# Kernel optimization log

Measured on AMD Instinct MI355X. Metric: run time of the kernel, lower is better.

The kernel has to match this reference:

```python
import math
import jax, jax.numpy as jnp
import numpy as np

B, IB, S, D = 8, 1024, 4096, 512
WINDOW = 1
SPARSITY = 2


def setup_inputs() -> dict:
    key = jax.random.key(0)
    ks = jax.random.split(key, 12)
    std = 1.0 / math.sqrt(D)
    std_b2s = 1.0 / math.sqrt(IB)
    return {
        "text_feature": jax.random.normal(ks[0], (B, S, D), jnp.float32),
        "image_feature": jax.random.normal(ks[1], (B, IB, D), jnp.float32),
        "Wq": jax.random.normal(ks[2], (D, D), jnp.float32) * std,
        "bq": jax.random.normal(ks[3], (D,), jnp.float32) * std,
        "Wk": jax.random.normal(ks[4], (D, D), jnp.float32) * std,
        "bk": jax.random.normal(ks[5], (D,), jnp.float32) * std,
        "Wv": jax.random.normal(ks[6], (D, D), jnp.float32) * std,
        "bv": jax.random.normal(ks[7], (D,), jnp.float32) * std,
        # torch Linear(in=IB, out=S): weight shape (S, IB)
        "Wb2s": jax.random.normal(ks[8], (S, IB), jnp.float32) * std_b2s,
        "bb2s": jax.random.normal(ks[9], (S,), jnp.float32) * std_b2s,
    }


def _banded_softmax_weights():
    # attention_mask[i, max(0,i-w):min(S,i+w+1)] = 1 ; since IB < S this is a
    # banded 0/1 matrix over (IB, IB), then row-softmax.
    i = jnp.arange(IB)[:, None]
    j = jnp.arange(IB)[None, :]
    mask = ((j >= i - WINDOW) & (j <= i + WINDOW)).astype(jnp.float32)
    return jax.nn.softmax(mask, axis=-1)  # (IB, IB)


def reference(text_feature, image_feature, Wq, bq, Wk, bk, Wv, bv, Wb2s, bb2s):
    d_k = text_feature.shape[-1]
    q = image_feature @ Wq.T + bq            # (B, IB, D)
    k = text_feature @ Wk.T + bk              # (B, S, D)
    v = text_feature @ Wv.T + bv              # (B, S, D)

    # batch-invariant sparse attention pattern: compute once, broadcast via einsum
    aw = _banded_softmax_weights()             # (IB, IB)
    aw = aw @ Wb2s.T + bb2s                    # (IB, S)
    num_nonzero = S // SPARSITY + 2 * WINDOW
    topk_scores, topk_idx = jax.lax.top_k(aw, num_nonzero)  # (IB, nnz)
    sparse = jnp.zeros((IB, S), aw.dtype).at[jnp.arange(IB)[:, None], topk_idx].set(topk_scores)

    out = jnp.einsum('is,bsd->bid', sparse, k)                       # (B, IB, D)
    out = jnp.einsum('bid,bjd->bij', q, out) / math.sqrt(d_k)        # (B, IB, IB)
    out = out @ Wb2s.T + bb2s                                        # (B, IB, S)
    out = jnp.einsum('bis,bsd->bid', jax.nn.softmax(out, axis=-1), v)  # (B, IB, D)
    return out
```

## Files before the change

### kernel.cpp

```cpp
#include <hip/hip_runtime.h>

#define B_  8
#define IB_ 1024
#define S_  4096
#define D_  512

typedef _Float16 f16;
typedef _Float16 f16x8 __attribute__((ext_vector_type(8)));
typedef _Float16 f16x4 __attribute__((ext_vector_type(4)));
typedef float    f32x4 __attribute__((ext_vector_type(4)));

__device__ __forceinline__ void gld_lds16(const f16* g, f16* l) {
  __builtin_amdgcn_global_load_lds(
      (const __attribute__((address_space(1))) void*)g,
      (__attribute__((address_space(3))) void*)l, 16, 0, 0);
}

__global__ __launch_bounds__(256) void gemm_bt(
    const f16* __restrict__ A, const f16* __restrict__ B,
    float* __restrict__ C32, f16* __restrict__ C16,
    int M, int N, int K, int lda, int ldb, int ksplit,
    long long sAb, long long sBb, long long sCb,
    const float* __restrict__ bias_row, const float* __restrict__ bias_col,
    float scale)
{
  __shared__ f16 ldsA[2][128 * 32];
  __shared__ f16 ldsB[2][128 * 32];
  const int tid  = threadIdx.x;
  const int lane = tid & 63;
  const int wave = tid >> 6;
  const int zb   = blockIdx.z / ksplit;
  const int ks   = blockIdx.z % ksplit;
  A += (size_t)zb * (size_t)sAb;
  B += (size_t)zb * (size_t)sBb;
  const int m0 = blockIdx.y * 128;
  const int n0 = blockIdx.x * 128;
  const int wm = wave >> 1, wn = wave & 1;

  f32x4 acc[4][4];
#pragma unroll
  for (int i = 0; i < 4; ++i)
#pragma unroll
    for (int j = 0; j < 4; ++j) acc[i][j] = (f32x4){0.f, 0.f, 0.f, 0.f};

  int aoff[4], boff[4];
  const int cl = lane >> 4;
#pragma unroll
  for (int r = 0; r < 4; ++r) {
    int rowa = wm * 64 + r * 16 + (lane & 15);
    aoff[r] = rowa * 32 + (cl ^ ((rowa >> 1) & 3)) * 8;
    int rowb = wn * 64 + r * 16 + (lane & 15);
    boff[r] = rowb * 32 + (cl ^ ((rowb >> 1) & 3)) * 8;
  }
  int srow[2], scg[2];
#pragma unroll
  for (int it = 0; it < 2; ++it) {
    int ch = wave * 64 + it * 256 + lane;
    srow[it] = ch >> 2;
    scg[it]  = (ch & 3) ^ ((srow[it] >> 1) & 3);
  }

#define STAGE(bf_, k0_)                                                        \
  do {                                                                         \
    _Pragma("unroll")                                                          \
    for (int it = 0; it < 2; ++it) {                                           \
      gld_lds16(A + (size_t)(m0 + srow[it]) * (size_t)lda +                    \
                    ((k0_) + scg[it] * 8),                                     \
                &ldsA[bf_][(wave * 64 + it * 256) * 8]);                       \
      gld_lds16(B + (size_t)(n0 + srow[it]) * (size_t)ldb +                    \
                    ((k0_) + scg[it] * 8),                                     \
                &ldsB[bf_][(wave * 64 + it * 256) * 8]);                       \
    }                                                                          \
  } while (0)

  const int Kc   = K / ksplit;
  const int kbeg = ks * Kc;
  const int nt   = Kc / 32;

  STAGE(0, kbeg);
  for (int t = 0; t < nt; ++t) {
    const int cur = t & 1;
    if (t + 1 < nt) {
      STAGE(cur ^ 1, kbeg + (t + 1) * 32);
      asm volatile("s_waitcnt vmcnt(4)" ::: "memory");
    } else {
      asm volatile("s_waitcnt vmcnt(0)" ::: "memory");
    }
    __builtin_amdgcn_s_barrier();
    __builtin_amdgcn_sched_barrier(0);
    f16x8 af[4], bf[4];
#pragma unroll
    for (int r = 0; r < 4; ++r) af[r] = *(const f16x8*)&ldsA[cur][aoff[r]];
#pragma unroll
    for (int r = 0; r < 4; ++r) bf[r] = *(const f16x8*)&ldsB[cur][boff[r]];
#pragma unroll
    for (int mr = 0; mr < 4; ++mr)
#pragma unroll
      for (int nr = 0; nr < 4; ++nr)
        acc[mr][nr] = __builtin_amdgcn_mfma_f32_16x16x32_f16(
            af[mr], bf[nr], acc[mr][nr], 0, 0, 0);
    __builtin_amdgcn_sched_barrier(0);
    __builtin_amdgcn_s_barrier();
    __builtin_amdgcn_sched_barrier(0);
  }
#undef STAGE

  const size_t cz = (ksplit > 1) ? (size_t)blockIdx.z : (size_t)zb;
  float* c32 = C32 ? C32 + cz * (size_t)sCb : nullptr;
  f16*   c16 = C16 ? C16 + cz * (size_t)sCb : nullptr;
#pragma unroll
  for (int mr = 0; mr < 4; ++mr) {
#pragma unroll
    for (int r = 0; r < 4; ++r) {
      int grow = m0 + wm * 64 + mr * 16 + (lane >> 4) * 4 + r;
      float brv = bias_row ? bias_row[grow] : 0.f;
#pragma unroll
      for (int nr = 0; nr < 4; ++nr) {
        int gcol = n0 + wn * 64 + nr * 16 + (lane & 15);
        float v = acc[mr][nr][r] * scale + brv +
                  (bias_col ? bias_col[gcol] : 0.f);
        if (c32) c32[(size_t)grow * N + gcol] = v;
        else     c16[(size_t)grow * N + gcol] = (f16)v;
      }
    }
  }
}

__global__ __launch_bounds__(256) void gemm_pt(
    const f16* __restrict__ Bt, const float* __restrict__ uarr,
    const float* __restrict__ inv2, const float* __restrict__ Acs,
    const float* __restrict__ bb2s, f16* __restrict__ parts)
{
  __shared__ f16 ldsB[2][128 * 32];
  __shared__ float cA[1024], cB[1024];
  const int tid  = threadIdx.x;
  const int lane = tid & 63;
  const int wave = tid >> 6;
  int id = (int)blockIdx.x;
  id = (id & 7) * 128 + (id >> 3);
  const int x  = id & 3;
  const int y  = (id >> 2) & 7;
  const int z  = id >> 5;
  const int zb = z >> 2, ks = z & 3;
  const int kbeg = ks * 1024;
  const int m0 = y * 128, n0 = x * 128;
  const int wm = wave >> 1, wn = wave & 1;
  const f16* B = Bt + (size_t)zb * ((size_t)D_ * S_);

  for (int i = tid; i < 1024; i += 256) {
    cA[i] = Acs[kbeg + i];
    cB[i] = bb2s[kbeg + i];
  }
  const int cl = lane >> 4;
  float u_[4], iv_[4];
#pragma unroll
  for (int r = 0; r < 4; ++r) {
    int row = zb * IB_ + m0 + wm * 64 + r * 16 + (lane & 15);
    u_[r]  = uarr[row];
    iv_[r] = inv2[row];
  }
  int boff[4];
#pragma unroll
  for (int r = 0; r < 4; ++r) {
    int rowb = wn * 64 + r * 16 + (lane & 15);
    boff[r] = rowb * 32 + (cl ^ ((rowb >> 1) & 3)) * 8;
  }
  int srow[2], scg[2];
#pragma unroll
  for (int it = 0; it < 2; ++it) {
    int ch = wave * 64 + it * 256 + lane;
    srow[it] = ch >> 2;
    scg[it]  = (ch & 3) ^ ((srow[it] >> 1) & 3);
  }
  f32x4 acc[4][4];
#pragma unroll
  for (int i = 0; i < 4; ++i)
#pragma unroll
    for (int j = 0; j < 4; ++j) acc[i][j] = (f32x4){0.f, 0.f, 0.f, 0.f};

#define STAGEB(bf_, k0_)                                                       \
  do {                                                                         \
    _Pragma("unroll")                                                          \
    for (int it = 0; it < 2; ++it) {                                           \
      gld_lds16(B + (size_t)(n0 + srow[it]) * (size_t)S_ +                     \
                    ((k0_) + scg[it] * 8),                                     \
                &ldsB[bf_][(wave * 64 + it * 256) * 8]);                       \
    }                                                                          \
  } while (0)

  __syncthreads();
  STAGEB(0, kbeg);
  for (int t = 0; t < 32; ++t) {
    const int cur = t & 1;
    if (t + 1 < 32) STAGEB(cur ^ 1, kbeg + (t + 1) * 32);
    const int kl = t * 32 + cl * 8;
    float a8[8], b8[8];
#pragma unroll
    for (int j = 0; j < 8; ++j) { a8[j] = cA[kl + j]; b8[j] = cB[kl + j]; }
    f16x8 af[4];
#pragma unroll
    for (int r = 0; r < 4; ++r)
#pragma unroll
      for (int j = 0; j < 8; ++j)
        af[r][j] = (f16)(__expf(fmaf(u_[r], a8[j], b8[j])) * iv_[r]);
    if (t + 1 < 32) asm volatile("s_waitcnt vmcnt(2)" ::: "memory");
    else            asm volatile("s_waitcnt vmcnt(0)" ::: "memory");
    __builtin_amdgcn_s_barrier();
    __builtin_amdgcn_sched_barrier(0);
    f16x8 bf[4];
#pragma unroll
    for (int r = 0; r < 4; ++r) bf[r] = *(const f16x8*)&ldsB[cur][boff[r]];
#pragma unroll
    for (int mr = 0; mr < 4; ++mr)
#pragma unroll
      for (int nr = 0; nr < 4; ++nr)
        acc[mr][nr] = __builtin_amdgcn_mfma_f32_16x16x32_f16(
            af[mr], bf[nr], acc[mr][nr], 0, 0, 0);
    __builtin_amdgcn_sched_barrier(0);
    __builtin_amdgcn_s_barrier();
    __builtin_amdgcn_sched_barrier(0);
  }
#undef STAGEB

  f16* cp = parts + (size_t)z * (size_t)(IB_ * D_);
#pragma unroll
  for (int mr = 0; mr < 4; ++mr) {
#pragma unroll
    for (int rr = 0; rr < 4; ++rr) {
      int grow = m0 + wm * 64 + mr * 16 + (lane >> 4) * 4 + rr;
#pragma unroll
      for (int nr = 0; nr < 4; ++nr) {
        int gcol = n0 + wn * 64 + nr * 16 + (lane & 15);
        cp[(size_t)grow * D_ + gcol] = (f16)acc[mr][nr][rr];
      }
    }
  }
}

__global__ __launch_bounds__(256) void reduce_ks4_f16(
    const f16x8* __restrict__ p, f16x8* __restrict__ o, unsigned n8)
{
  const unsigned pb8 = (IB_ * D_) / 8;
  unsigned i = blockIdx.x * 256u + threadIdx.x;
  const unsigned stride = gridDim.x * 256u;
  for (; i < n8; i += stride) {
    unsigned g = i / pb8, r = i - g * pb8;
    size_t base = ((size_t)g * 4u) * pb8 + r;
    float acc[8] = {0.f, 0.f, 0.f, 0.f, 0.f, 0.f, 0.f, 0.f};
#pragma unroll
    for (int ks = 0; ks < 4; ++ks) {
      f16x8 v = p[base + (size_t)ks * pb8];
#pragma unroll
      for (int j = 0; j < 8; ++j) acc[j] += (float)v[j];
    }
    f16x8 h;
#pragma unroll
    for (int j = 0; j < 8; ++j) h[j] = (f16)acc[j];
    o[i] = h;
  }
}

__global__ __launch_bounds__(256) void reduce_ks2_bias(
    const f16x8* __restrict__ p, const float* __restrict__ bias,
    float4* __restrict__ o, unsigned n8)
{
  unsigned i = blockIdx.x * 256u + threadIdx.x;
  const unsigned stride = gridDim.x * 256u;
  for (; i < n8; i += stride) {
    f16x8 a = p[i];
    f16x8 b = p[i + (size_t)n8];
    const int c0 = (int)((i * 8u) & (D_ - 1));
    float4 lo, hi;
    lo.x = (float)a[0] + (float)b[0] + bias[c0 + 0];
    lo.y = (float)a[1] + (float)b[1] + bias[c0 + 1];
    lo.z = (float)a[2] + (float)b[2] + bias[c0 + 2];
    lo.w = (float)a[3] + (float)b[3] + bias[c0 + 3];
    hi.x = (float)a[4] + (float)b[4] + bias[c0 + 4];
    hi.y = (float)a[5] + (float)b[5] + bias[c0 + 5];
    hi.z = (float)a[6] + (float)b[6] + bias[c0 + 6];
    hi.w = (float)a[7] + (float)b[7] + bias[c0 + 7];
    o[(size_t)i * 2]     = lo;
    o[(size_t)i * 2 + 1] = hi;
  }
}

__global__ __launch_bounds__(256) void cvt_f32_to_f16(
    const float* __restrict__ in, f16* __restrict__ out, unsigned n)
{
  unsigned i = (blockIdx.x * 256u + threadIdx.x) * 4u;
  if (i >= n) return;
  const float4 v = *(const float4*)(in + i);
  f16x4 h;
  h[0] = (f16)v.x; h[1] = (f16)v.y; h[2] = (f16)v.z; h[3] = (f16)v.w;
  *(f16x4*)(out + i) = h;
}

__global__ __launch_bounds__(256) void transpose_text(
    const float* __restrict__ in, f16* __restrict__ out)
{
  __shared__ float t[32][65];
  const int b = blockIdx.z;
  const int s0 = blockIdx.x * 64, d0 = blockIdx.y * 32;
  const int dx = threadIdx.x & 31;
  const int sy = threadIdx.x >> 5;
  const float* ip = in + ((size_t)b * S_ + s0) * D_ + d0;
#pragma unroll
  for (int j = 0; j < 8; ++j) {
    int sl = j * 8 + sy;
    t[dx][sl] = ip[(size_t)sl * D_ + dx];
  }
  __syncthreads();
  const int sx = threadIdx.x & 63;
  const int dy = threadIdx.x >> 6;
  f16* op = out + ((size_t)b * D_ + d0) * S_ + s0;
#pragma unroll
  for (int j = 0; j < 8; ++j) {
    int dl = j * 4 + dy;
    op[(size_t)dl * S_ + sx] = (f16)t[dl][sx];
  }
}

__global__ __launch_bounds__(256) void rowsum_kernel(
    const float* __restrict__ W, float* __restrict__ out)
{
  int s = blockIdx.x;
  const float* row = W + (size_t)s * IB_;
  float acc = 0.f;
  for (int j = threadIdx.x; j < IB_; j += 256) acc += row[j];
  __shared__ float red[4];
#pragma unroll
  for (int o = 32; o >= 1; o >>= 1) acc += __shfl_xor(acc, o);
  if ((threadIdx.x & 63) == 0) red[threadIdx.x >> 6] = acc;
  __syncthreads();
  if (threadIdx.x == 0) out[s] = red[0] + red[1] + red[2] + red[3];
}

__device__ __forceinline__ unsigned fkey(float x) {
  unsigned u = __float_as_uint(x);
  return (u & 0x80000000u) ? ~u : (u | 0x80000000u);
}

__global__ __launch_bounds__(256) void prep_mu(
    const float* __restrict__ Acs, const float* __restrict__ bb2s,
    float* __restrict__ muk, float* __restrict__ rhat)
{
  __shared__ float vals[S_];
  __shared__ unsigned hist[256];
  __shared__ unsigned sprefix;
  __shared__ int srem;
  __shared__ float rred[4];
  const float e1 = 2.71828182845904523536f;
  const float Z = 3.f * e1 + (float)(IB_ - 3);
  const float alpha = 1.f / Z;
  for (int s = threadIdx.x; s < S_; s += 256)
    vals[s] = alpha * Acs[s] + bb2s[s];
  if (threadIdx.x == 0) { sprefix = 0u; srem = S_ / 2 + 2; }
  __syncthreads();
  for (int shift = 24; shift >= 0; shift -= 8) {
    hist[threadIdx.x] = 0u;
    __syncthreads();
    unsigned pfx = sprefix;
    unsigned himask = (shift == 24) ? 0u : (0xFFFFFFFFu << (shift + 8));
    for (int s = threadIdx.x; s < S_; s += 256) {
      unsigned key = fkey(vals[s]);
      if ((key & himask) == (pfx & himask))
        atomicAdd(&hist[(key >> shift) & 255u], 1u);
    }
    __syncthreads();
    if (threadIdx.x == 0) {
      int rem = srem;
      unsigned acc = 0;
      int b = 255;
      for (; b > 0; --b) {
        unsigned c = hist[b];
        if (acc + c >= (unsigned)rem) break;
        acc += c;
      }
      sprefix = pfx | ((unsigned)b << shift);
      srem = rem - (int)acc;
    }
    __syncthreads();
  }
  const unsigned T = sprefix;
  float myrs = 0.f;
  for (int s = threadIdx.x; s < S_; s += 256) {
    float v = vals[s];
    bool keep = fkey(v) >= T;
    muk[s] = keep ? v : 0.f;
    if (keep) myrs += v;
  }
#pragma unroll
  for (int o = 32; o >= 1; o >>= 1) myrs += __shfl_xor(myrs, o);
  if ((threadIdx.x & 63) == 0) rred[threadIdx.x >> 6] = myrs;
  __syncthreads();
  if (threadIdx.x == 0) rhat[0] = rred[0] + rred[1] + rred[2] + rred[3];
}

__global__ __launch_bounds__(256) void that_partial(
    const float* __restrict__ text, const float* __restrict__ muk,
    float* __restrict__ tp)
{
  const int d = blockIdx.x * 256 + threadIdx.x;
  const int c = blockIdx.y;
  const int b = blockIdx.z;
  const float* tb = text + ((size_t)b * S_ + (size_t)c * 128) * D_ + d;
  float acc = 0.f;
  for (int s = 0; s < 128; ++s) {
    float m = muk[c * 128 + s];
    if (m != 0.f) acc += m * tb[(size_t)s * D_];
  }
  tp[((size_t)b * 32 + c) * D_ + d] = acc;
}

__global__ __launch_bounds__(256) void tt_reduce(
    const float* __restrict__ tp, float* __restrict__ tt)
{
  const int d = blockIdx.x * 256 + threadIdx.x;
  const int b = blockIdx.y;
  float acc = 0.f;
#pragma unroll
  for (int c = 0; c < 32; ++c) acc += tp[((size_t)b * 32 + c) * D_ + d];
  tt[(size_t)b * D_ + d] = acc;
}

__global__ __launch_bounds__(256) void mhat2_kernel(
    const float* __restrict__ tt, const float* __restrict__ Wk,
    const float* __restrict__ bk, const float* __restrict__ rhat,
    float* __restrict__ mh)
{
  __shared__ float tl[B_ * D_];
  const int t = threadIdx.x;
  for (int i = t; i < B_ * D_; i += 256) tl[i] = tt[i];
  __syncthreads();
  const int r = blockIdx.x;
  const int lane = t & 63, wave = t >> 6;
  const float* wr = Wk + (size_t)r * D_;
  float w[8];
#pragma unroll
  for (int j = 0; j < 8; ++j) w[j] = wr[lane + 64 * j];
  const float bkr = bk[r] * rhat[0];
#pragma unroll
  for (int bb = 0; bb < 2; ++bb) {
    const int b = wave * 2 + bb;
    float acc = 0.f;
#pragma unroll
    for (int j = 0; j < 8; ++j) acc += w[j] * tl[b * D_ + lane + 64 * j];
#pragma unroll
    for (int o = 32; o >= 1; o >>= 1) acc += __shfl_xor(acc, o);
    if (lane == 0) mh[b * D_ + r] = acc + bkr;
  }
}

__global__ __launch_bounds__(256) void ypart_kernel(
    const float* __restrict__ Wq, const float* __restrict__ mh,
    float* __restrict__ yp)
{
  __shared__ float ms[B_ * 64];
  const int t = threadIdx.x;
  const int d = blockIdx.x * 256 + t;
  const int c = blockIdx.y;
  for (int i = t; i < B_ * 64; i += 256) {
    int b = i >> 6, rr = i & 63;
    ms[i] = mh[b * D_ + c * 64 + rr];
  }
  __syncthreads();
  float acc[8] = {0.f, 0.f, 0.f, 0.f, 0.f, 0.f, 0.f, 0.f};
  for (int rr = 0; rr < 64; ++rr) {
    float wv = Wq[(size_t)(c * 64 + rr) * D_ + d];
#pragma unroll
    for (int b = 0; b < 8; ++b) acc[b] += wv * ms[b * 64 + rr];
  }
#pragma unroll
  for (int b = 0; b < 8; ++b)
    yp[((size_t)c * 8 + b) * D_ + d] = acc[b];
}

__global__ __launch_bounds__(256) void yred_kernel(
    const float* __restrict__ yp, float* __restrict__ y)
{
  const int d = blockIdx.x * 256 + threadIdx.x;
  const int b = blockIdx.y;
  float acc = 0.f;
#pragma unroll
  for (int c = 0; c < 8; ++c) acc += yp[((size_t)c * 8 + b) * D_ + d];
  y[(size_t)b * D_ + d] = acc;
}

__global__ __launch_bounds__(256) void cb_kernel(
    const float* __restrict__ bq, const float* __restrict__ mh,
    float* __restrict__ cb)
{
  const int lane = threadIdx.x & 63, wave = threadIdx.x >> 6;
#pragma unroll
  for (int bb = 0; bb < 2; ++bb) {
    const int b = wave * 2 + bb;
    float acc = 0.f;
#pragma unroll
    for (int j = 0; j < 8; ++j) {
      int k = lane + 64 * j;
      acc += bq[k] * mh[b * D_ + k];
    }
#pragma unroll
    for (int o = 32; o >= 1; o >>= 1) acc += __shfl_xor(acc, o);
    if (lane == 0) cb[b] = acc;
  }
}

__global__ __launch_bounds__(256) void u_kernel(
    const float* __restrict__ img, const float* __restrict__ y,
    const float* __restrict__ cb, float scl, float* __restrict__ u)
{
  const int lane = threadIdx.x & 63, wave = threadIdx.x >> 6;
  const int row = blockIdx.x * 4 + wave;
  const int b = row >> 10;
  const float* ir = img + (size_t)row * D_;
  const float* yb = y + (size_t)b * D_;
  float acc = 0.f;
#pragma unroll
  for (int j = 0; j < 8; ++j) {
    int d = lane + 64 * j;
    acc += ir[d] * yb[d];
  }
#pragma unroll
  for (int o = 32; o >= 1; o >>= 1) acc += __shfl_xor(acc, o);
  if (lane == 0) u[row] = (acc + cb[b]) * scl;
}

__global__ __launch_bounds__(256) void pstat_kernel(
    const float* __restrict__ uarr, const float* __restrict__ Acs,
    const float* __restrict__ bb2s, float* __restrict__ inv2)
{
  const int row = blockIdx.x;
  const int t = threadIdx.x;
  __shared__ float red[4];
  const float u = uarr[row];
  float v[16];
  float mx = -3.4e38f;
#pragma unroll
  for (int j = 0; j < 16; ++j) {
    int s = t + 256 * j;
    v[j] = fmaf(u, Acs[s], bb2s[s]);
    mx = fmaxf(mx, v[j]);
  }
#pragma unroll
  for (int o = 32; o >= 1; o >>= 1) mx = fmaxf(mx, __shfl_xor(mx, o));
  if ((t & 63) == 0) red[t >> 6] = mx;
  __syncthreads();
  mx = fmaxf(fmaxf(red[0], red[1]), fmaxf(red[2], red[3]));
  __syncthreads();
  float sum = 0.f;
#pragma unroll
  for (int j = 0; j < 16; ++j) sum += __expf(v[j] - mx);
#pragma unroll
  for (int o = 32; o >= 1; o >>= 1) sum += __shfl_xor(sum, o);
  if ((t & 63) == 0) red[t >> 6] = sum;
  __syncthreads();
  if (t == 0) {
    float Zs = red[0] + red[1] + red[2] + red[3];
    inv2[row] = __expf(-mx) / Zs;
  }
}

extern "C" void kernel_launch(void* const* d_in, const int* in_sizes, int n_in,
                              void* d_out, int out_size, void* d_ws, size_t ws_size,
                              hipStream_t stream)
{
  const float* text = (const float*)d_in[0];
  const float* img  = (const float*)d_in[1];
  const float* Wq   = (const float*)d_in[2];
  const float* bq   = (const float*)d_in[3];
  const float* Wk   = (const float*)d_in[4];
  const float* bk   = (const float*)d_in[5];
  const float* Wv   = (const float*)d_in[6];
  const float* bv   = (const float*)d_in[7];
  const float* Wb2s = (const float*)d_in[8];
  const float* bb2s = (const float*)d_in[9];
  float* outp = (float*)d_out;
  char* ws = (char*)d_ws;

  const long long ID = (long long)IB_ * D_;
  const size_t MB = 1048576ull;

  const size_t NEED = 96 * MB;
  if (ws_size < NEED) return;

  f16*   textT   = (f16*)(ws + 0);
  f16*   pt16    = (f16*)(ws + 32 * MB);
  f16*   partsPT = (f16*)(ws + 40 * MB);
  f16*   partsO  = (f16*)(ws + 72 * MB);
  f16*   wv16    = (f16*)(ws + 88 * MB);
  const size_t SB = 89 * MB;
  float* Acs  = (float*)(ws + SB);
  float* muk  = (float*)(ws + SB + 16384);
  float* tp   = (float*)(ws + SB + 32768);
  float* tt   = (float*)(ws + SB + 557056);
  float* mh   = (float*)(ws + SB + 573440);
  float* rhat = (float*)(ws + SB + 589824);
  float* yp   = (float*)(ws + SB + 593920);
  float* y    = (float*)(ws + SB + 724992);
  float* cb   = (float*)(ws + SB + 741376);
  float* u    = (float*)(ws + SB + 745472);
  float* inv2 = (float*)(ws + SB + 778240);

  dim3 blk(256);
  const float scl = 0.04419417382415922f;

  rowsum_kernel<<<S_, blk, 0, stream>>>(Wb2s, Acs);
  prep_mu<<<1, blk, 0, stream>>>(Acs, bb2s, muk, rhat);
  that_partial<<<dim3(2, 32, B_), blk, 0, stream>>>(text, muk, tp);
  tt_reduce<<<dim3(2, B_), blk, 0, stream>>>(tp, tt);
  mhat2_kernel<<<512, blk, 0, stream>>>(tt, Wk, bk, rhat, mh);
  ypart_kernel<<<dim3(2, 8), blk, 0, stream>>>(Wq, mh, yp);
  yred_kernel<<<dim3(2, B_), blk, 0, stream>>>(yp, y);
  cb_kernel<<<1, blk, 0, stream>>>(bq, mh, cb);
  u_kernel<<<(B_ * IB_) / 4, blk, 0, stream>>>(img, y, cb, scl, u);
  pstat_kernel<<<B_ * IB_, blk, 0, stream>>>(u, Acs, bb2s, inv2);
  transpose_text<<<dim3(S_/64, D_/32, B_), blk, 0, stream>>>(text, textT);
  gemm_pt<<<1024, blk, 0, stream>>>(textT, u, inv2, Acs, bb2s, partsPT);
  reduce_ks4_f16<<<1024, blk, 0, stream>>>(
      (const f16x8*)partsPT, (f16x8*)pt16, (unsigned)((B_ * ID) / 8));
  cvt_f32_to_f16<<<(D_*D_)/1024, blk, 0, stream>>>(Wv, wv16, D_*D_);
  gemm_bt<<<dim3(D_/128, (B_*IB_)/128, 2), blk, 0, stream>>>(
      pt16, wv16, nullptr, partsO, B_*IB_, D_, D_, D_, D_, 2,
      0, 0, (long long)B_ * ID, nullptr, nullptr, 1.f);
  reduce_ks2_bias<<<1024, blk, 0, stream>>>(
      (const f16x8*)partsO, bv, (float4*)outp, (unsigned)((B_ * ID) / 8));
}
```

Baseline: 217.1 us.

## Retile gemm_pt to 64x256 with shared exp-computed A tile in LDS

```diff
diff --git a/kernel.cpp b/kernel.cpp
--- a/kernel.cpp
+++ b/kernel.cpp
@@ -131,43 +131,45 @@
     const float* __restrict__ inv2, const float* __restrict__ Acs,
     const float* __restrict__ bb2s, f16* __restrict__ parts)
 {
-  __shared__ f16 ldsB[2][128 * 32];
-  __shared__ float cA[1024], cB[1024];
+  __shared__ f16 ldsA[64 * 32];
+  __shared__ f16 ldsB[2][256 * 32];
+  __shared__ float cA2[1024], cB2[1024];
   const int tid  = threadIdx.x;
   const int lane = tid & 63;
   const int wave = tid >> 6;
   int id = (int)blockIdx.x;
   id = (id & 7) * 128 + (id >> 3);
-  const int x  = id & 3;
-  const int y  = (id >> 2) & 7;
-  const int z  = id >> 5;
-  const int zb = z >> 2, ks = z & 3;
+  const int zb = id >> 7;
+  const int rem = id & 127;
+  const int mt = rem >> 3;
+  const int x  = (rem >> 2) & 1;
+  const int ks = rem & 3;
   const int kbeg = ks * 1024;
-  const int m0 = y * 128, n0 = x * 128;
-  const int wm = wave >> 1, wn = wave & 1;
+  const int m0 = mt * 64, n0 = x * 256;
   const f16* B = Bt + (size_t)zb * ((size_t)D_ * S_);
 
+  const float L2E = 1.44269504088896340736f;
   for (int i = tid; i < 1024; i += 256) {
-    cA[i] = Acs[kbeg + i];
-    cB[i] = bb2s[kbeg + i];
-  }
+    cA2[i] = Acs[kbeg + i] * L2E;
+    cB2[i] = bb2s[kbeg + i] * L2E;
+  }
+  const int srowA = tid >> 2;
+  const int scgA  = tid & 3;
+  const int spcA  = scgA ^ ((srowA >> 1) & 3);
+  const float u_  = uarr[zb * IB_ + m0 + srowA];
+  const float iv_ = inv2[zb * IB_ + m0 + srowA];
   const int cl = lane >> 4;
-  float u_[4], iv_[4];
+  int aoff[4], boff[4];
 #pragma unroll
   for (int r = 0; r < 4; ++r) {
-    int row = zb * IB_ + m0 + wm * 64 + r * 16 + (lane & 15);
-    u_[r]  = uarr[row];
-    iv_[r] = inv2[row];
-  }
-  int boff[4];
-#pragma unroll
-  for (int r = 0; r < 4; ++r) {
-    int rowb = wn * 64 + r * 16 + (lane & 15);
+    int rowa = r * 16 + (lane & 15);
+    aoff[r] = rowa * 32 + (cl ^ ((rowa >> 1) & 3)) * 8;
+    int rowb = wave * 64 + r * 16 + (lane & 15);
     boff[r] = rowb * 32 + (cl ^ ((rowb >> 1) & 3)) * 8;
   }
-  int srow[2], scg[2];
-#pragma unroll
-  for (int it = 0; it < 2; ++it) {
+  int srow[4], scg[4];
+#pragma unroll
+  for (int it = 0; it < 4; ++it) {
     int ch = wave * 64 + it * 256 + lane;
     srow[it] = ch >> 2;
     scg[it]  = (ch & 3) ^ ((srow[it] >> 1) & 3);
@@ -181,7 +183,7 @@
 #define STAGEB(bf_, k0_)                                                       \
   do {                                                                         \
     _Pragma("unroll")                                                          \
-    for (int it = 0; it < 2; ++it) {                                           \
+    for (int it = 0; it < 4; ++it) {                                           \
       gld_lds16(B + (size_t)(n0 + srow[it]) * (size_t)S_ +                     \
                     ((k0_) + scg[it] * 8),                                     \
                 &ldsB[bf_][(wave * 64 + it * 256) * 8]);                       \
@@ -193,23 +195,29 @@
   for (int t = 0; t < 32; ++t) {
     const int cur = t & 1;
     if (t + 1 < 32) STAGEB(cur ^ 1, kbeg + (t + 1) * 32);
-    const int kl = t * 32 + cl * 8;
-    float a8[8], b8[8];
-#pragma unroll
-    for (int j = 0; j < 8; ++j) { a8[j] = cA[kl + j]; b8[j] = cB[kl + j]; }
-    f16x8 af[4];
-#pragma unroll
-    for (int r = 0; r < 4; ++r)
-#pragma unroll
-      for (int j = 0; j < 8; ++j)
-        af[r][j] = (f16)(__expf(fmaf(u_[r], a8[j], b8[j])) * iv_[r]);
-    if (t + 1 < 32) asm volatile("s_waitcnt vmcnt(2)" ::: "memory");
+    {
+      const int kl = t * 32 + scgA * 8;
+      f16x8 hp;
+#pragma unroll
+      for (int j = 0; j < 8; ++j) {
+        float e = exp2f(fmaf(u_, cA2[kl + j], cB2[kl + j])) * iv_;
+        hp[j] = (f16)e;
+      }
+      *(f16x8*)&ldsA[srowA * 32 + spcA * 8] = hp;
+    }
+    asm volatile("s_waitcnt lgkmcnt(0)" ::: "memory");
+    __builtin_amdgcn_sched_barrier(0);
+    if (t + 1 < 32) asm volatile("s_waitcnt vmcnt(4)" ::: "memory");
     else            asm volatile("s_waitcnt vmcnt(0)" ::: "memory");
     __builtin_amdgcn_s_barrier();
     __builtin_amdgcn_sched_barrier(0);
-    f16x8 bf[4];
+    f16x8 af[4], bf[4];
+#pragma unroll
+    for (int r = 0; r < 4; ++r) af[r] = *(const f16x8*)&ldsA[aoff[r]];
 #pragma unroll
     for (int r = 0; r < 4; ++r) bf[r] = *(const f16x8*)&ldsB[cur][boff[r]];
+    asm volatile("s_waitcnt lgkmcnt(0)" ::: "memory");
+    __builtin_amdgcn_sched_barrier(0);
 #pragma unroll
     for (int mr = 0; mr < 4; ++mr)
 #pragma unroll
@@ -222,15 +230,15 @@
   }
 #undef STAGEB
 
-  f16* cp = parts + (size_t)z * (size_t)(IB_ * D_);
+  f16* cp = parts + (size_t)(zb * 4 + ks) * (size_t)(IB_ * D_);
 #pragma unroll
   for (int mr = 0; mr < 4; ++mr) {
 #pragma unroll
     for (int rr = 0; rr < 4; ++rr) {
-      int grow = m0 + wm * 64 + mr * 16 + (lane >> 4) * 4 + rr;
+      int grow = m0 + mr * 16 + (lane >> 4) * 4 + rr;
 #pragma unroll
       for (int nr = 0; nr < 4; ++nr) {
-        int gcol = n0 + wn * 64 + nr * 16 + (lane & 15);
+        int gcol = n0 + wave * 64 + nr * 16 + (lane & 15);
         cp[(size_t)grow * D_ + gcol] = (f16)acc[mr][nr][rr];
       }
     }
```

Measured after the change: 217.2 us. No clear change (+0.0%).
